# Optimization experiments

Measured on AMD Instinct MI355X. Metric: run time of the kernel, lower is better.

Reference implementation:

```python
import jax, jax.numpy as jnp
import numpy as np

N_NODES = 131072
N_EDGES = 2097152
IN_DIM = 256
HID = 128
BATCH = 32
MAX_COM = 10
C = 1.0          # Poincare ball curvature
EPS = 1e-5
MIN_NORM = 1e-15


def _row_norm(x):
    return jnp.sqrt(jnp.clip(jnp.sum(x * x, axis=-1, keepdims=True), MIN_NORM, None))


def proj(x, c=C):
    # clip points inside the Poincare ball of radius (1-eps)/sqrt(c)
    norm = _row_norm(x)
    maxnorm = (1.0 - EPS) / jnp.sqrt(c)
    return jnp.where(norm > maxnorm, x / norm * maxnorm, x)


def logmap0(x, c=C):
    sqrt_c = jnp.sqrt(c)
    norm = _row_norm(x)
    arg = jnp.clip(sqrt_c * norm, None, 1.0 - 1e-7)
    return x * jnp.arctanh(arg) / (sqrt_c * norm)


def expmap0(u, c=C):
    sqrt_c = jnp.sqrt(c)
    norm = _row_norm(u)
    return u * jnp.tanh(sqrt_c * norm) / (sqrt_c * norm)


def gcn_layer(x, W, b, src, dst, n_nodes):
    # support = x @ W ; out[dst] += support[src] ; out += b  (raw adjacency spmm)
    support = x @ W
    agg = jax.ops.segment_sum(support[src], dst, num_segments=n_nodes)
    return agg + b


def setup_inputs() -> dict:
    key = jax.random.key(0)
    ks = jax.random.split(key, 8)
    x = jax.random.normal(ks[0], (N_NODES, IN_DIM), dtype=jnp.float32) * 0.1
    src = jax.random.randint(ks[1], (N_EDGES,), 0, N_NODES)
    dst = jax.random.randint(ks[2], (N_EDGES,), 0, N_NODES)
    seg_ids = jax.random.randint(ks[3], (N_NODES,), 0, BATCH * MAX_COM)
    W1 = jax.random.normal(ks[4], (IN_DIM, HID), dtype=jnp.float32) / np.sqrt(IN_DIM)
    b1 = jnp.zeros((HID,), dtype=jnp.float32)
    W2 = jax.random.normal(ks[5], (HID, HID), dtype=jnp.float32) / np.sqrt(HID)
    b2 = jnp.zeros((HID,), dtype=jnp.float32)
    return {"x": x, "src": src, "dst": dst, "seg_ids": seg_ids,
            "W1": W1, "b1": b1, "W2": W2, "b2": b2,
            "batch_size": BATCH, "max_comments": MAX_COM}


def reference(x, src, dst, seg_ids, W1, b1, W2, b2, batch_size, max_comments):
    n_nodes = x.shape[0]
    h = jnp.tanh(gcn_layer(x, W1, b1, src, dst, n_nodes))
    h = jnp.tanh(gcn_layer(h, W2, b2, src, dst, n_nodes))
    # tangent-space coordinates
    h = logmap0(proj(h))
    # per-(batch, comment) subgraph mean pooling == segment mean
    n_seg = batch_size * max_comments
    sums = jax.ops.segment_sum(h, seg_ids, num_segments=n_seg)
    counts = jax.ops.segment_sum(jnp.ones((n_nodes,), h.dtype), seg_ids, num_segments=n_seg)
    agg = sums / jnp.maximum(counts, 1.0)[:, None]   # empty segments -> zeros (padding)
    agg = proj(expmap0(agg))
    return agg.reshape(batch_size, max_comments, -1)
```

## Files before the change

### kernel.cpp

```cpp
#include <hip/hip_runtime.h>
#include <hip/hip_bf16.h>

#define IN_DIM 256
#define HID    128
#define NSEG   320
#define MAXNORM 0.99999

#define G      8
#define NGRP   16384
#define NPAN   32
#define PANSH  12
#define NKEY   (NGRP * NPAN)

typedef short bf16x8 __attribute__((ext_vector_type(8)));
typedef float f32x4  __attribute__((ext_vector_type(4)));

static __device__ __forceinline__ ushort f2b(float f) {
    uint u = __builtin_bit_cast(uint, f);
    uint r = 0x7FFFu + ((u >> 16) & 1u);
    return (ushort)((u + r) >> 16);
}
static __device__ __forceinline__ float b2f_lo(uint v) {
    return __builtin_bit_cast(float, v << 16);
}
static __device__ __forceinline__ float b2f_hi(uint v) {
    return __builtin_bit_cast(float, v & 0xFFFF0000u);
}

__global__ void count_edges_k(const int* __restrict__ src, const int* __restrict__ dst,
                              int* __restrict__ counts, int n) {
    int e = blockIdx.x * 256 + threadIdx.x;
    if (e < n) {
        int key = ((dst[e] >> 3) << 5) | (src[e] >> PANSH);
        atomicAdd(&counts[key], 1);
    }
}

__global__ void scan_block_k(const int* __restrict__ in, int* __restrict__ out,
                             int* __restrict__ partials) {
    __shared__ int sh[256];
    int tid = threadIdx.x;
    int base = blockIdx.x * 1024 + tid * 4;
    int4 v = *(const int4*)&in[base];
    int s = v.x + v.y + v.z + v.w;
    sh[tid] = s;
    __syncthreads();
#pragma unroll
    for (int off = 1; off < 256; off <<= 1) {
        int t = (tid >= off) ? sh[tid - off] : 0;
        __syncthreads();
        sh[tid] += t;
        __syncthreads();
    }
    int excl = sh[tid] - s;
    int4 o;
    o.x = excl; o.y = excl + v.x; o.z = o.y + v.y; o.w = o.z + v.z;
    *(int4*)&out[base] = o;
    if (tid == 255) partials[blockIdx.x] = sh[255];
}

__global__ void scan_partials_k(int* __restrict__ partials, int n) {
    __shared__ int sh[1024];
    int tid = threadIdx.x;
    int v = (tid < n) ? partials[tid] : 0;
    sh[tid] = v;
    __syncthreads();
    for (int off = 1; off < blockDim.x; off <<= 1) {
        int t = (tid >= off) ? sh[tid - off] : 0;
        __syncthreads();
        sh[tid] += t;
        __syncthreads();
    }
    if (tid < n) partials[tid] = sh[tid] - v;
}

__global__ void add_base_k(int* __restrict__ offsets, const int* __restrict__ partials, int n) {
    int g = blockIdx.x * 256 + threadIdx.x;
    if (g < n) offsets[g] += partials[g >> 10];
}

__global__ void fill_edges_k(const int* __restrict__ src, const int* __restrict__ dst,
                             const int* __restrict__ offsets, int* __restrict__ cursor,
                             uint* __restrict__ packed, int n) {
    int e = blockIdx.x * 256 + threadIdx.x;
    if (e < n) {
        int s = src[e], d = dst[e];
        int key = ((d >> 3) << 5) | (s >> PANSH);
        int pos = atomicAdd(&cursor[key], 1);
        packed[offsets[key] + pos] = (uint)s | ((uint)(d & 7) << 28);
    }
}

__global__ void extract_goff_k(const int* __restrict__ offsets, int* __restrict__ goff, int E) {
    int g = blockIdx.x * 256 + threadIdx.x;
    if (g < NGRP) goff[g] = offsets[g << 5];
    if (g == NGRP) goff[g] = E;
}

__global__ void prep_wt_k(const float* __restrict__ w1, const float* __restrict__ w2,
                          ushort* __restrict__ w1t, ushort* __restrict__ w2t) {
    int id = blockIdx.x * 256 + threadIdx.x;
    if (id < 32768) {
        int n = id >> 8, k = id & 255;
        w1t[n * 256 + k] = f2b(w1[k * 128 + n]);
    } else {
        int id2 = id - 32768;
        int n = id2 >> 7, k = id2 & 127;
        w2t[n * 128 + k] = f2b(w2[k * 128 + n]);
    }
}

template<bool AF32>
__global__ __launch_bounds__(256) void gemm_k(const void* __restrict__ Ap,
                                              const ushort* __restrict__ BT,
                                              ushort* __restrict__ C, int K) {
    __shared__ __align__(16) char As[16384];
    __shared__ __align__(16) char Bs[16384];
    const int tid = threadIdx.x;
    const int lane = tid & 63;
    const int wid = tid >> 6;
    const int wr = wid >> 1, wc = wid & 1;
    const int row0 = blockIdx.x * 128;
    f32x4 acc[4][4] = {};

    for (int k0 = 0; k0 < K; k0 += 64) {
        if (AF32) {
            const float* A = (const float*)Ap;
#pragma unroll
            for (int it = 0; it < 8; ++it) {
                int id = tid + it * 256;
                int r = id >> 4, c4 = (id & 15) * 4;
                float4 v = *(const float4*)&A[(size_t)(row0 + r) * K + k0 + c4];
                ushort4 h;
                h.x = f2b(v.x); h.y = f2b(v.y); h.z = f2b(v.z); h.w = f2b(v.w);
                *(ushort4*)(As + ((r * 128 + c4 * 2) ^ ((r & 7) << 4))) = h;
            }
        } else {
            const ushort* A = (const ushort*)Ap;
#pragma unroll
            for (int it = 0; it < 4; ++it) {
                int id = tid + it * 256;
                int r = id >> 3, c8 = (id & 7) * 8;
                bf16x8 v = *(const bf16x8*)&A[(size_t)(row0 + r) * K + k0 + c8];
                *(bf16x8*)(As + ((r * 128 + c8 * 2) ^ ((r & 7) << 4))) = v;
            }
        }
#pragma unroll
        for (int it = 0; it < 4; ++it) {
            int id = tid + it * 256;
            int n = id >> 3, c8 = (id & 7) * 8;
            bf16x8 v = *(const bf16x8*)&BT[(size_t)n * K + k0 + c8];
            *(bf16x8*)(Bs + ((n * 128 + c8 * 2) ^ ((n & 7) << 4))) = v;
        }
        __syncthreads();
#pragma unroll
        for (int kc = 0; kc < 2; ++kc) {
            bf16x8 af[4], bfr[4];
            int kb = (kc * 32 + (lane >> 4) * 8) * 2;
#pragma unroll
            for (int i = 0; i < 4; ++i) {
                int r = wr * 64 + i * 16 + (lane & 15);
                af[i] = *(const bf16x8*)(As + ((r * 128 + kb) ^ ((r & 7) << 4)));
                int n = wc * 64 + i * 16 + (lane & 15);
                bfr[i] = *(const bf16x8*)(Bs + ((n * 128 + kb) ^ ((n & 7) << 4)));
            }
#pragma unroll
            for (int i = 0; i < 4; ++i)
#pragma unroll
                for (int j = 0; j < 4; ++j)
                    acc[i][j] = __builtin_amdgcn_mfma_f32_16x16x32_bf16(
                        af[i], bfr[j], acc[i][j], 0, 0, 0);
        }
        __syncthreads();
    }
#pragma unroll
    for (int i = 0; i < 4; ++i)
#pragma unroll
        for (int j = 0; j < 4; ++j)
#pragma unroll
            for (int r = 0; r < 4; ++r) {
                int row = row0 + wr * 64 + i * 16 + (lane >> 4) * 4 + r;
                int col = wc * 64 + j * 16 + (lane & 15);
                C[(size_t)row * 128 + col] = f2b(acc[i][j][r]);
            }
}

template<bool POOL>
__global__ __launch_bounds__(256, 8) void gather_grp_k(
    const uint* __restrict__ sup, const int* __restrict__ goff,
    const uint* __restrict__ packed, const float* __restrict__ bias,
    const int* __restrict__ seg_ids, uint* __restrict__ h1,
    float* __restrict__ sums, int* __restrict__ seg_cnt) {
    __shared__ float lds[4][G * 128];
    const int wslot = threadIdx.x >> 6;
    const int lane  = threadIdx.x & 63;
    float* acc = &lds[wslot][0];
    const int wave = blockIdx.x * 4 + wslot;
    float2 bv = *(const float2*)&bias[2 * lane];

    for (int sweep = 0; sweep < 2; ++sweep) {
        const int g = wave * 2 + sweep;
#pragma unroll
        for (int n = 0; n < G; ++n)
            *(float2*)&acc[n * 128 + 2 * lane] = float2{0.f, 0.f};

        int base = goff[g];
        int cnt  = goff[g + 1] - base;
        int j = 0;
        while (j < cnt) {
            int rem = cnt - j; if (rem > 64) rem = 64;
            uint pe = 0;
            if (lane < rem) pe = packed[base + j + lane];
            int t = 0;
            for (; t + 16 <= rem; t += 16) {
                uint r[16];
#pragma unroll
                for (int u = 0; u < 16; ++u) {
                    uint p = __builtin_amdgcn_readlane(pe, t + u);
                    uint s = p & 0xFFFFFFu;
                    r[u] = sup[(size_t)s * 64 + lane];
                }
#pragma unroll
                for (int u = 0; u < 16; ++u) {
                    uint p = __builtin_amdgcn_readlane(pe, t + u);
                    uint l = p >> 28;
                    float2 a = *(float2*)&acc[l * 128 + 2 * lane];
                    a.x += b2f_lo(r[u]); a.y += b2f_hi(r[u]);
                    *(float2*)&acc[l * 128 + 2 * lane] = a;
                }
            }
            for (; t < rem; ++t) {
                uint p = __builtin_amdgcn_readlane(pe, t);
                uint s = p & 0xFFFFFFu;
                uint l = p >> 28;
                uint v = sup[(size_t)s * 64 + lane];
                float2 a = *(float2*)&acc[l * 128 + 2 * lane];
                a.x += b2f_lo(v); a.y += b2f_hi(v);
                *(float2*)&acc[l * 128 + 2 * lane] = a;
            }
            j += rem;
        }
#pragma unroll
        for (int n = 0; n < G; ++n) {
            int node = g * G + n;
            float2 a = *(float2*)&acc[n * 128 + 2 * lane];
            float hx = tanhf(a.x + bv.x), hy = tanhf(a.y + bv.y);
            if (!POOL) {
                h1[(size_t)node * 64 + lane] = ((uint)f2b(hy) << 16) | (uint)f2b(hx);
            } else {
                float ss = hx * hx + hy * hy;
#pragma unroll
                for (int o = 32; o > 0; o >>= 1) ss += __shfl_xor(ss, o);
                double rr = sqrt((double)fmaxf(ss, 1e-15f));
                double m = fmin(rr, MAXNORM);
                float f = (float)(atanh(m) / rr);
                int seg = seg_ids[node];
                atomicAdd(&sums[seg * 128 + 2 * lane], hx * f);
                atomicAdd(&sums[seg * 128 + 2 * lane + 1], hy * f);
                if (lane == 0) atomicAdd(&seg_cnt[seg], 1);
            }
        }
    }
}

__global__ __launch_bounds__(64) void finalize_k(const float* __restrict__ sums,
                                                 const int* __restrict__ seg_cnt,
                                                 float* __restrict__ out) {
    int seg = blockIdx.x;
    int lane = threadIdx.x;
    float c = fmaxf((float)seg_cnt[seg], 1.0f);
    float ux = sums[seg * 128 + 2 * lane] / c;
    float uy = sums[seg * 128 + 2 * lane + 1] / c;
    float ss = ux * ux + uy * uy;
#pragma unroll
    for (int o = 32; o > 0; o >>= 1) ss += __shfl_xor(ss, o);
    double r = sqrt((double)fmaxf(ss, 1e-15f));
    double t = tanh(r);
    double fac = t / r;
    if (t > MAXNORM) fac = MAXNORM / r;
    float f = (float)fac;
    out[seg * 128 + 2 * lane] = ux * f;
    out[seg * 128 + 2 * lane + 1] = uy * f;
}

extern "C" void kernel_launch(void* const* d_in, const int* in_sizes, int n_in,
                              void* d_out, int out_size, void* d_ws, size_t ws_size,
                              hipStream_t stream) {
    const float* x   = (const float*)d_in[0];
    const int* src   = (const int*)d_in[1];
    const int* dst   = (const int*)d_in[2];
    const int* segid = (const int*)d_in[3];
    const float* W1  = (const float*)d_in[4];
    const float* b1  = (const float*)d_in[5];
    const float* W2  = (const float*)d_in[6];
    const float* b2  = (const float*)d_in[7];
    float* out       = (float*)d_out;

    const int N = in_sizes[3];
    const int E = in_sizes[1];

    char* ws = (char*)d_ws;
    ushort* supA   = (ushort*)(ws);
    uint*   supA32 = (uint*)supA;
    uint*   h1u    = (uint*)(ws + 33554432);
    ushort* h1     = (ushort*)h1u;
    uint* packed   = (uint*)(ws + 67108864);
    int* goff      = (int*)(ws + 75497472);
    float* sums    = (float*)(ws + 75563264);
    int* seg_cnt   = (int*)(ws + 75727104);
    ushort* w1t    = (ushort*)(ws + 75728384);
    ushort* w2t    = (ushort*)(ws + 75793920);
    int* counts    = (int*)(ws);
    int* offsets   = (int*)(ws + 2097152);
    int* cursor    = (int*)(ws + 4194304);
    int* partials  = (int*)(ws + 6291456);

    hipMemsetAsync(counts, 0, (size_t)NKEY * 4, stream);
    hipMemsetAsync(cursor, 0, (size_t)NKEY * 4, stream);
    hipMemsetAsync(sums, 0, (size_t)NSEG * 128 * 4, stream);
    hipMemsetAsync(seg_cnt, 0, (size_t)NSEG * 4, stream);

    const int eblocks = (E + 255) / 256;

    prep_wt_k<<<192, 256, 0, stream>>>(W1, W2, w1t, w2t);

    count_edges_k<<<eblocks, 256, 0, stream>>>(src, dst, counts, E);
    scan_block_k<<<NKEY / 1024, 256, 0, stream>>>(counts, offsets, partials);
    scan_partials_k<<<1, NKEY / 1024, 0, stream>>>(partials, NKEY / 1024);
    add_base_k<<<NKEY / 256, 256, 0, stream>>>(offsets, partials, NKEY);
    fill_edges_k<<<eblocks, 256, 0, stream>>>(src, dst, offsets, cursor, packed, E);
    extract_goff_k<<<(NGRP + 256) / 256, 256, 0, stream>>>(offsets, goff, E);

    gemm_k<true><<<N / 128, 256, 0, stream>>>(x, w1t, supA, IN_DIM);
    gather_grp_k<false><<<2048, 256, 0, stream>>>(supA32, goff, packed, b1, segid,
                                                  h1u, sums, seg_cnt);

    gemm_k<false><<<N / 128, 256, 0, stream>>>(h1, w2t, supA, HID);
    gather_grp_k<true><<<2048, 256, 0, stream>>>(supA32, goff, packed, b2, segid,
                                                 h1u, sums, seg_cnt);

    finalize_k<<<NSEG, 64, 0, stream>>>(sums, seg_cnt, out);
}
```

Baseline: 597.7 us.

## Split support into column halves and gather per wave over 32-node groups

Restructures the sparse aggregation. The GEMM now writes the support matrix as two 64-column halves, and the edge sort key becomes (32-node dst group, src panel of 16384, dst within group). The new gather kernel makes two passes, one per half, and each wave sweeps the 8 src panels in order while issuing throwaway loads of the next panel slice to warm the cache. It also accumulates runs of edges with the same destination in registers before flushing to LDS. Pooling moves out into its own kernel that re-reads h2. This aims at better cache locality for the random src reads, in exchange for more passes over the edges, an extra h2 round trip, and a larger workspace.

```diff
diff --git a/kernel.cpp b/kernel.cpp
--- a/kernel.cpp
+++ b/kernel.cpp
@@ -6,11 +6,10 @@
 #define NSEG   320
 #define MAXNORM 0.99999
 
-#define G      8
-#define NGRP   16384
-#define NPAN   32
-#define PANSH  12
-#define NKEY   (NGRP * NPAN)
+#define NPAN   8
+#define PANSH  14
+#define NWAVE  4096
+#define NKEY   (NWAVE * 256)
 
 typedef short bf16x8 __attribute__((ext_vector_type(8)));
 typedef float f32x4  __attribute__((ext_vector_type(4)));
@@ -26,12 +25,16 @@
 static __device__ __forceinline__ float b2f_hi(uint v) {
     return __builtin_bit_cast(float, v & 0xFFFF0000u);
 }
+static __device__ __forceinline__ float b2fu(ushort u) {
+    return __builtin_bit_cast(float, (uint)u << 16);
+}
 
 __global__ void count_edges_k(const int* __restrict__ src, const int* __restrict__ dst,
                               int* __restrict__ counts, int n) {
     int e = blockIdx.x * 256 + threadIdx.x;
     if (e < n) {
-        int key = ((dst[e] >> 3) << 5) | (src[e] >> PANSH);
+        int d = dst[e];
+        int key = ((d >> 5) << 8) | ((src[e] >> PANSH) << 5) | (d & 31);
         atomicAdd(&counts[key], 1);
     }
 }
@@ -85,16 +88,16 @@
     int e = blockIdx.x * 256 + threadIdx.x;
     if (e < n) {
         int s = src[e], d = dst[e];
-        int key = ((d >> 3) << 5) | (s >> PANSH);
+        int key = ((d >> 5) << 8) | ((s >> PANSH) << 5) | (d & 31);
         int pos = atomicAdd(&cursor[key], 1);
-        packed[offsets[key] + pos] = (uint)s | ((uint)(d & 7) << 28);
-    }
-}
-
-__global__ void extract_goff_k(const int* __restrict__ offsets, int* __restrict__ goff, int E) {
-    int g = blockIdx.x * 256 + threadIdx.x;
-    if (g < NGRP) goff[g] = offsets[g << 5];
-    if (g == NGRP) goff[g] = E;
+        packed[offsets[key] + pos] = (uint)s | ((uint)(d & 31) << 20);
+    }
+}
+
+__global__ void extract_goff2_k(const int* __restrict__ offsets, int* __restrict__ goff2, int E) {
+    int i = blockIdx.x * 256 + threadIdx.x;
+    if (i < NWAVE * NPAN) goff2[i] = offsets[(i >> 3) * 256 + (i & 7) * 32];
+    if (i == NWAVE * NPAN) goff2[i] = E;
 }
 
 __global__ void prep_wt_k(const float* __restrict__ w1, const float* __restrict__ w2,
@@ -113,7 +116,8 @@
 template<bool AF32>
 __global__ __launch_bounds__(256) void gemm_k(const void* __restrict__ Ap,
                                               const ushort* __restrict__ BT,
-                                              ushort* __restrict__ C, int K) {
+                                              ushort* __restrict__ CLo,
+                                              ushort* __restrict__ CHi, int K) {
     __shared__ __align__(16) char As[16384];
     __shared__ __align__(16) char Bs[16384];
     const int tid = threadIdx.x;
@@ -173,6 +177,7 @@
         }
         __syncthreads();
     }
+    ushort* Cb = wc ? CHi : CLo;
 #pragma unroll
     for (int i = 0; i < 4; ++i)
 #pragma unroll
@@ -180,87 +185,104 @@
 #pragma unroll
             for (int r = 0; r < 4; ++r) {
                 int row = row0 + wr * 64 + i * 16 + (lane >> 4) * 4 + r;
-                int col = wc * 64 + j * 16 + (lane & 15);
-                C[(size_t)row * 128 + col] = f2b(acc[i][j][r]);
-            }
-}
-
-template<bool POOL>
-__global__ __launch_bounds__(256, 8) void gather_grp_k(
-    const uint* __restrict__ sup, const int* __restrict__ goff,
-    const uint* __restrict__ packed, const float* __restrict__ bias,
-    const int* __restrict__ seg_ids, uint* __restrict__ h1,
-    float* __restrict__ sums, int* __restrict__ seg_cnt) {
-    __shared__ float lds[4][G * 128];
-    const int wslot = threadIdx.x >> 6;
-    const int lane  = threadIdx.x & 63;
-    float* acc = &lds[wslot][0];
-    const int wave = blockIdx.x * 4 + wslot;
-    float2 bv = *(const float2*)&bias[2 * lane];
-
-    for (int sweep = 0; sweep < 2; ++sweep) {
-        const int g = wave * 2 + sweep;
-#pragma unroll
-        for (int n = 0; n < G; ++n)
-            *(float2*)&acc[n * 128 + 2 * lane] = float2{0.f, 0.f};
-
-        int base = goff[g];
-        int cnt  = goff[g + 1] - base;
-        int j = 0;
-        while (j < cnt) {
-            int rem = cnt - j; if (rem > 64) rem = 64;
-            uint pe = 0;
-            if (lane < rem) pe = packed[base + j + lane];
-            int t = 0;
-            for (; t + 16 <= rem; t += 16) {
-                uint r[16];
-#pragma unroll
-                for (int u = 0; u < 16; ++u) {
-                    uint p = __builtin_amdgcn_readlane(pe, t + u);
-                    uint s = p & 0xFFFFFFu;
-                    r[u] = sup[(size_t)s * 64 + lane];
+                int col = j * 16 + (lane & 15);
+                Cb[(size_t)row * 64 + col] = f2b(acc[i][j][r]);
+            }
+}
+
+__global__ __launch_bounds__(256) void gather_ph_k(
+    const ushort* __restrict__ supLo, const ushort* __restrict__ supHi,
+    const uint* __restrict__ packed, const int* __restrict__ goff2,
+    const float* __restrict__ bias, ushort* __restrict__ hout) {
+    __shared__ float accs[4][2048];
+    const int ws = threadIdx.x >> 6;
+    const int lane = threadIdx.x & 63;
+    const int w = blockIdx.x * 4 + ws;
+    float* accw = accs[ws];
+    const int slice = (blockIdx.x >> 3) & 127;
+
+    for (int pass = 0; pass < 2; ++pass) {
+        const ushort* sup = pass ? supHi : supLo;
+        for (int i = lane; i < 2048; i += 64) accw[i] = 0.f;
+
+        uint k0, k1, k2, k3;
+        {
+            const uint4* pb = (const uint4*)sup + slice * 1024 + ws * 256 + lane;
+            uint4 a = pb[0], b = pb[64], c = pb[128], d = pb[192];
+            k0 = a.x ^ a.y ^ a.z ^ a.w; k1 = b.x ^ b.y ^ b.z ^ b.w;
+            k2 = c.x ^ c.y ^ c.z ^ c.w; k3 = d.x ^ d.y ^ d.z ^ d.w;
+            asm volatile("" :: "v"(k0), "v"(k1), "v"(k2), "v"(k3));
+        }
+        for (int p = 0; p < NPAN; ++p) {
+            if (p < NPAN - 1) {
+                const uint4* pb = (const uint4*)sup + (size_t)(p + 1) * 131072
+                                  + slice * 1024 + ws * 256 + lane;
+                uint4 a = pb[0], b = pb[64], c = pb[128], d = pb[192];
+                k0 = a.x ^ a.y ^ a.z ^ a.w; k1 = b.x ^ b.y ^ b.z ^ b.w;
+                k2 = c.x ^ c.y ^ c.z ^ c.w; k3 = d.x ^ d.y ^ d.z ^ d.w;
+            }
+            int a = __builtin_amdgcn_readfirstlane(goff2[w * NPAN + p]);
+            int b = __builtin_amdgcn_readfirstlane(goff2[w * NPAN + p + 1]);
+            float accv = 0.f;
+            int prev = -1;
+            int e = a;
+            for (; e + 8 <= b; e += 8) {
+                uint pes[8]; ushort vs[8];
+#pragma unroll
+                for (int t = 0; t < 8; ++t) pes[t] = packed[e + t];
+#pragma unroll
+                for (int t = 0; t < 8; ++t)
+                    vs[t] = sup[(size_t)(pes[t] & 0xFFFFFu) * 64 + lane];
+#pragma unroll
+                for (int t = 0; t < 8; ++t) {
+                    int dl = (int)(pes[t] >> 20);
+                    if (dl != prev) {
+                        if (prev >= 0) accw[prev * 64 + lane] += accv;
+                        accv = 0.f; prev = dl;
+                    }
+                    accv += b2fu(vs[t]);
                 }
-#pragma unroll
-                for (int u = 0; u < 16; ++u) {
-                    uint p = __builtin_amdgcn_readlane(pe, t + u);
-                    uint l = p >> 28;
-                    float2 a = *(float2*)&acc[l * 128 + 2 * lane];
-                    a.x += b2f_lo(r[u]); a.y += b2f_hi(r[u]);
-                    *(float2*)&acc[l * 128 + 2 * lane] = a;
+            }
+            for (; e < b; ++e) {
+                uint pe = packed[e];
+                int dl = (int)(pe >> 20);
+                if (dl != prev) {
+                    if (prev >= 0) accw[prev * 64 + lane] += accv;
+                    accv = 0.f; prev = dl;
                 }
-            }
-            for (; t < rem; ++t) {
-                uint p = __builtin_amdgcn_readlane(pe, t);
-                uint s = p & 0xFFFFFFu;
-                uint l = p >> 28;
-                uint v = sup[(size_t)s * 64 + lane];
-                float2 a = *(float2*)&acc[l * 128 + 2 * lane];
-                a.x += b2f_lo(v); a.y += b2f_hi(v);
-                *(float2*)&acc[l * 128 + 2 * lane] = a;
-            }
-            j += rem;
-        }
-#pragma unroll
-        for (int n = 0; n < G; ++n) {
-            int node = g * G + n;
-            float2 a = *(float2*)&acc[n * 128 + 2 * lane];
-            float hx = tanhf(a.x + bv.x), hy = tanhf(a.y + bv.y);
-            if (!POOL) {
-                h1[(size_t)node * 64 + lane] = ((uint)f2b(hy) << 16) | (uint)f2b(hx);
-            } else {
-                float ss = hx * hx + hy * hy;
-#pragma unroll
-                for (int o = 32; o > 0; o >>= 1) ss += __shfl_xor(ss, o);
-                double rr = sqrt((double)fmaxf(ss, 1e-15f));
-                double m = fmin(rr, MAXNORM);
-                float f = (float)(atanh(m) / rr);
-                int seg = seg_ids[node];
-                atomicAdd(&sums[seg * 128 + 2 * lane], hx * f);
-                atomicAdd(&sums[seg * 128 + 2 * lane + 1], hy * f);
-                if (lane == 0) atomicAdd(&seg_cnt[seg], 1);
-            }
-        }
-    }
+                accv += b2fu(sup[(size_t)(pe & 0xFFFFFu) * 64 + lane]);
+            }
+            if (prev >= 0) accw[prev * 64 + lane] += accv;
+            asm volatile("" :: "v"(k0), "v"(k1), "v"(k2), "v"(k3));
+        }
+        float bv = bias[pass * 64 + lane];
+#pragma unroll 4
+        for (int n = 0; n < 32; ++n) {
+            int node = w * 32 + n;
+            float th = tanhf(accw[n * 64 + lane] + bv);
+            hout[(size_t)node * 128 + pass * 64 + lane] = f2b(th);
+        }
+    }
+}
+
+__global__ __launch_bounds__(256) void pool_k(
+    const uint* __restrict__ h2u, const int* __restrict__ seg_ids,
+    float* __restrict__ sums, int* __restrict__ seg_cnt, int n_nodes) {
+    int node = (blockIdx.x << 2) | (threadIdx.x >> 6);
+    if (node >= n_nodes) return;
+    int lane = threadIdx.x & 63;
+    uint v = h2u[(size_t)node * 64 + lane];
+    float hx = b2f_lo(v), hy = b2f_hi(v);
+    float ss = hx * hx + hy * hy;
+#pragma unroll
+    for (int o = 32; o > 0; o >>= 1) ss += __shfl_xor(ss, o);
+    double rr = sqrt((double)fmaxf(ss, 1e-15f));
+    double m = fmin(rr, MAXNORM);
+    float f = (float)(atanh(m) / rr);
+    int seg = seg_ids[node];
+    atomicAdd(&sums[seg * 128 + 2 * lane], hx * f);
+    atomicAdd(&sums[seg * 128 + 2 * lane + 1], hy * f);
+    if (lane == 0) atomicAdd(&seg_cnt[seg], 1);
 }
 
 __global__ __launch_bounds__(64) void finalize_k(const float* __restrict__ sums,
@@ -300,20 +322,21 @@
     const int E = in_sizes[1];
 
     char* ws = (char*)d_ws;
-    ushort* supA   = (ushort*)(ws);
-    uint*   supA32 = (uint*)supA;
-    uint*   h1u    = (uint*)(ws + 33554432);
-    ushort* h1     = (ushort*)h1u;
-    uint* packed   = (uint*)(ws + 67108864);
-    int* goff      = (int*)(ws + 75497472);
-    float* sums    = (float*)(ws + 75563264);
-    int* seg_cnt   = (int*)(ws + 75727104);
-    ushort* w1t    = (ushort*)(ws + 75728384);
-    ushort* w2t    = (ushort*)(ws + 75793920);
-    int* counts    = (int*)(ws);
-    int* offsets   = (int*)(ws + 2097152);
-    int* cursor    = (int*)(ws + 4194304);
-    int* partials  = (int*)(ws + 6291456);
+    ushort* supLo  = (ushort*)(ws);
+    ushort* supHi  = (ushort*)(ws + 16777216);
+    ushort* h1     = (ushort*)(ws + 33554432);
+    ushort* h2     = (ushort*)(ws + 67108864);
+    uint*   h2u    = (uint*)h2;
+    uint* packed   = (uint*)(ws + 100663296);
+    int* goff2     = (int*)(ws + 109051904);
+    float* sums    = (float*)(ws + 110100480);
+    int* seg_cnt   = (int*)(ws + 110264320);
+    ushort* w1t    = (ushort*)(ws + 110265600);
+    ushort* w2t    = (ushort*)(ws + 110331136);
+    int* counts    = (int*)(ws + 33554432);
+    int* offsets   = (int*)(ws + 37748736);
+    int* cursor    = (int*)(ws + 41943040);
+    int* partials  = (int*)(ws + 67108864);
 
     hipMemsetAsync(counts, 0, (size_t)NKEY * 4, stream);
     hipMemsetAsync(cursor, 0, (size_t)NKEY * 4, stream);
@@ -326,18 +349,17 @@
 
     count_edges_k<<<eblocks, 256, 0, stream>>>(src, dst, counts, E);
     scan_block_k<<<NKEY / 1024, 256, 0, stream>>>(counts, offsets, partials);
-    scan_partials_k<<<1, NKEY / 1024, 0, stream>>>(partials, NKEY / 1024);
+    scan_partials_k<<<1, 1024, 0, stream>>>(partials, NKEY / 1024);
     add_base_k<<<NKEY / 256, 256, 0, stream>>>(offsets, partials, NKEY);
     fill_edges_k<<<eblocks, 256, 0, stream>>>(src, dst, offsets, cursor, packed, E);
-    extract_goff_k<<<(NGRP + 256) / 256, 256, 0, stream>>>(offsets, goff, E);
-
-    gemm_k<true><<<N / 128, 256, 0, stream>>>(x, w1t, supA, IN_DIM);
-    gather_grp_k<false><<<2048, 256, 0, stream>>>(supA32, goff, packed, b1, segid,
-                                                  h1u, sums, seg_cnt);
-
-    gemm_k<false><<<N / 128, 256, 0, stream>>>(h1, w2t, supA, HID);
-    gather_grp_k<true><<<2048, 256, 0, stream>>>(supA32, goff, packed, b2, segid,
-                                                 h1u, sums, seg_cnt);
-
+    extract_goff2_k<<<(NWAVE * NPAN + 256) / 256, 256, 0, stream>>>(offsets, goff2, E);
+
+    gemm_k<true><<<N / 128, 256, 0, stream>>>(x, w1t, supLo, supHi, IN_DIM);
+    gather_ph_k<<<1024, 256, 0, stream>>>(supLo, supHi, packed, goff2, b1, h1);
+
+    gemm_k<false><<<N / 128, 256, 0, stream>>>(h1, w2t, supLo, supHi, HID);
+    gather_ph_k<<<1024, 256, 0, stream>>>(supLo, supHi, packed, goff2, b2, h2);
+
+    pool_k<<<N / 4, 256, 0, stream>>>(h2u, segid, sums, seg_cnt, N);
     finalize_k<<<NSEG, 64, 0, stream>>>(sums, seg_cnt, out);
 }
```

After: 792.3 us. 32.5% more time.
